# Performance work log

Measured on AMD Instinct MI355X. Metric: run time of the kernel, lower is better.

Reference implementation:

```python
import jax, jax.numpy as jnp
import numpy as np

N, E = 20000, 320000
NODE_DIM, EDGE_DIM, EMB, HEADS, HIDDEN, OUT = 128, 16, 128, 4, 512, 64
NEG_SLOPE = 0.2


def _gatv2(x, src0, dst0, ea, Wl, bl, Wr, br, We, att, bias):
    """PyG GATv2Conv (concat=True, add_self_loops=True, fill_value='mean')."""
    n = x.shape[0]
    e = src0.shape[0]
    H, C = att.shape
    # self loops; self-loop edge_attr = mean of incoming edge_attr per node (0 if none)
    cnt = jax.ops.segment_sum(jnp.ones((e,), x.dtype), dst0, num_segments=n)
    loop_attr = jax.ops.segment_sum(ea, dst0, num_segments=n) / jnp.maximum(cnt, 1.0)[:, None]
    loops = jnp.arange(n, dtype=src0.dtype)
    src = jnp.concatenate([src0, loops])
    dst = jnp.concatenate([dst0, loops])
    ea_full = jnp.concatenate([ea, loop_attr], axis=0)
    xl = (x @ Wl + bl).reshape(n, H, C)   # source transform
    xr = (x @ Wr + br).reshape(n, H, C)   # target transform
    ef = (ea_full @ We).reshape(-1, H, C)  # edge transform (no bias in PyG)
    s = jax.nn.leaky_relu(xl[src] + xr[dst] + ef, NEG_SLOPE)  # [E', H, C]
    logits = jnp.einsum('ehc,hc->eh', s, att)
    # scatter-softmax over incoming edges of each dst node (stable)
    mx = jax.ops.segment_max(logits, dst, num_segments=n)
    num = jnp.exp(logits - mx[dst])
    den = jax.ops.segment_sum(num, dst, num_segments=n)
    alpha = num / (den[dst] + 1e-16)
    out = jax.ops.segment_sum(alpha[:, :, None] * xl[src], dst, num_segments=n)
    return out.reshape(n, H * C) + bias


def _lin(key, fan_in, fan_out, dt=jnp.float32):
    return jax.random.normal(key, (fan_in, fan_out), dt) * (1.0 / np.sqrt(fan_in))


def setup_inputs() -> dict:
    key = jax.random.key(0)
    ks = jax.random.split(key, 24)
    HC = HEADS * EMB
    inp = {
        'x': jax.random.normal(ks[0], (N, NODE_DIM), jnp.float32),
        'edge_index': jax.random.randint(ks[1], (2, E), 0, N, jnp.int64),
        'edge_attr': jax.random.normal(ks[2], (E, EDGE_DIM), jnp.float32),
        # GATv2 layer 1
        'Wl1': _lin(ks[3], NODE_DIM, HC), 'bl1': jnp.zeros((HC,), jnp.float32),
        'Wr1': _lin(ks[4], NODE_DIM, HC), 'br1': jnp.zeros((HC,), jnp.float32),
        'We1': _lin(ks[5], EDGE_DIM, HC),
        'att1': jax.random.normal(ks[6], (HEADS, EMB), jnp.float32) * (1.0 / np.sqrt(EMB)),
        'bias1': jnp.zeros((HC,), jnp.float32),
        # GATv2 layer 2
        'Wl2': _lin(ks[7], HC, HC), 'bl2': jnp.zeros((HC,), jnp.float32),
        'Wr2': _lin(ks[8], HC, HC), 'br2': jnp.zeros((HC,), jnp.float32),
        'We2': _lin(ks[9], EDGE_DIM, HC),
        'att2': jax.random.normal(ks[10], (HEADS, EMB), jnp.float32) * (1.0 / np.sqrt(EMB)),
        'bias2': jnp.zeros((HC,), jnp.float32),
        # decoder MLP
        'Wd1': _lin(ks[11], HC, HIDDEN), 'bd1': jnp.zeros((HIDDEN,), jnp.float32),
        'Wd2': _lin(ks[12], HIDDEN, OUT), 'bd2': jnp.zeros((OUT,), jnp.float32),
    }
    return inp


def reference(x, edge_index, edge_attr,
              Wl1, bl1, Wr1, br1, We1, att1, bias1,
              Wl2, bl2, Wr2, br2, We2, att2, bias2,
              Wd1, bd1, Wd2, bd2):
    src, dst = edge_index[0], edge_index[1]
    h = _gatv2(x, src, dst, edge_attr, Wl1, bl1, Wr1, br1, We1, att1, bias1)
    h = _gatv2(h, src, dst, edge_attr, Wl2, bl2, Wr2, br2, We2, att2, bias2)
    q = jax.nn.relu(h @ Wd1 + bd1) @ Wd2 + bd2
    return q
```

## Files before the change

kernel.cpp:

```cpp
#include <hip/hip_runtime.h>
#include <hip/hip_fp16.h>

typedef _Float16 half8 __attribute__((ext_vector_type(8)));
typedef _Float16 half4 __attribute__((ext_vector_type(4)));
typedef _Float16 half2v __attribute__((ext_vector_type(2)));
typedef float f32x4 __attribute__((ext_vector_type(4)));

#if __has_builtin(__builtin_amdgcn_fdot2)
#define FDOT2(a, b, c) __builtin_amdgcn_fdot2((a), (b), (c), false)
#else
static __device__ __forceinline__ float FDOT2(half2v a, half2v b, float c) {
  return (float)a[0] * (float)b[0] + (float)a[1] * (float)b[1] + c;
}
#endif
#define H2(v8, p) ((half2v){(v8)[2 * (p)], (v8)[2 * (p) + 1]})

#define GLOAD_LDS16(gp, lp)                                                        \
  __builtin_amdgcn_global_load_lds(                                                \
      (const __attribute__((address_space(1))) void*)(gp),                         \
      (__attribute__((address_space(3))) void*)(lp), 16, 0, 0)

template <int CTRL>
__device__ __forceinline__ float dpp_add16(float x) {
  int y = __builtin_amdgcn_update_dpp(0, __float_as_int(x), CTRL, 0xf, 0xf, true);
  return x + __int_as_float(y);
}
__device__ __forceinline__ float rowsum16(float x) {
  x = dpp_add16<0x128>(x);
  x = dpp_add16<0x124>(x);
  x = dpp_add16<0x122>(x);
  x = dpp_add16<0x121>(x);
  return x;
}

__global__ void prep_kernel(const float* __restrict__ x, _Float16* __restrict__ x16, int nx,
                            const float* __restrict__ Wl1, const float* __restrict__ Wr1,
                            _Float16* __restrict__ WlrT1,
                            const float* __restrict__ Wl2, const float* __restrict__ Wr2,
                            _Float16* __restrict__ WlrT2,
                            const float* __restrict__ Wd1, _Float16* __restrict__ WdT1,
                            const float* __restrict__ Wd2, _Float16* __restrict__ WdT2,
                            const float* __restrict__ We1, _Float16* __restrict__ WeF1,
                            const float* __restrict__ We2, _Float16* __restrict__ WeF2,
                            const float* __restrict__ att1, _Float16* __restrict__ att16_1,
                            const float* __restrict__ att2, _Float16* __restrict__ att16_2,
                            const int* __restrict__ dst0, int* __restrict__ deg, int E) {
  int i = blockIdx.x * 256 + threadIdx.x;
  if (i < nx) { x16[i] = (_Float16)x[i]; return; }
  i -= nx;
  if (i < 1024 * 128) {
    int n = i >> 7, k = i & 127;
    float v = (n < 512) ? Wl1[(size_t)k * 512 + n] : Wr1[(size_t)k * 512 + (n - 512)];
    WlrT1[i] = (_Float16)v; return;
  }
  i -= 1024 * 128;
  if (i < 1024 * 512) {
    int n = i >> 9, k = i & 511;
    float v = (n < 512) ? Wl2[(size_t)k * 512 + n] : Wr2[(size_t)k * 512 + (n - 512)];
    WlrT2[i] = (_Float16)v; return;
  }
  i -= 1024 * 512;
  if (i < 512 * 512) { int n = i >> 9, k = i & 511; WdT1[i] = (_Float16)Wd1[(size_t)k * 512 + n]; return; }
  i -= 512 * 512;
  if (i < 64 * 512)  { int n = i >> 9, k = i & 511; WdT2[i] = (_Float16)Wd2[(size_t)k * 64 + n]; return; }
  i -= 64 * 512;
  if (i < 512 * 16) {
    int k = i & 15, c = (i >> 4) & 15, g = i >> 8;
    WeF1[i] = (_Float16)We1[(size_t)k * 512 + g * 16 + c]; return;
  }
  i -= 512 * 16;
  if (i < 512 * 16) {
    int k = i & 15, c = (i >> 4) & 15, g = i >> 8;
    WeF2[i] = (_Float16)We2[(size_t)k * 512 + g * 16 + c]; return;
  }
  i -= 512 * 16;
  if (i < 512)       { att16_1[i] = (_Float16)att1[i]; return; }
  i -= 512;
  if (i < 512)       { att16_2[i] = (_Float16)att2[i]; return; }
  i -= 512;
  if (i < E)         { atomicAdd(&deg[dst0[i]], 1); return; }
}

__global__ __launch_bounds__(1024) void scan_kernel(const int* __restrict__ deg, int* __restrict__ offs, int N) {
  __shared__ int part[1024];
  int t = threadIdx.x;
  int chunk = (N + 1023) / 1024;
  int b = t * chunk, e = min(b + chunk, N);
  int s = 0;
  for (int i = b; i < e; i++) s += deg[i] + 1;
  part[t] = s;
  __syncthreads();
  for (int off = 1; off < 1024; off <<= 1) {
    int v = (t >= off) ? part[t - off] : 0;
    __syncthreads();
    part[t] += v;
    __syncthreads();
  }
  int run = (t == 0) ? 0 : part[t - 1];
  for (int i = b; i < e; i++) { offs[i] = run; run += deg[i] + 1; }
  if (t == 1023) offs[N] = part[1023];
}

__global__ void csr_fill_kernel(const int* __restrict__ src0, const int* __restrict__ dst0,
                                const float* __restrict__ ea,
                                const int* __restrict__ offs, const int* __restrict__ deg,
                                int* __restrict__ cnt, int* __restrict__ csr_src,
                                _Float16* __restrict__ eas, int E, int N) {
  int i = blockIdx.x * 256 + threadIdx.x;
  if (i < 64) {
    if (i < 16) csr_src[E + N + i] = 0;
#pragma unroll
    for (int k = 0; k < 16; k++) eas[(size_t)(E + N + i) * 16 + k] = (_Float16)0.f;
  }
  if (i < E) {
    int d = dst0[i];
    int p = offs[d] + atomicAdd(&cnt[d], 1);
    csr_src[p] = src0[i];
    const float* s = ea + (size_t)i * 16;
    half8 h0, h1;
#pragma unroll
    for (int k = 0; k < 8; k++) { h0[k] = (_Float16)s[k]; h1[k] = (_Float16)s[k + 8]; }
    *(half8*)(eas + (size_t)p * 16) = h0;
    *(half8*)(eas + (size_t)p * 16 + 8) = h1;
  } else if (i < E + N) {
    int v = i - E;
    csr_src[offs[v] + deg[v]] = v;
  }
}

__global__ void loop_attr_kernel(const int* __restrict__ offs, const int* __restrict__ deg,
                                 _Float16* __restrict__ eas, int N) {
  int wid = (blockIdx.x * 256 + threadIdx.x) >> 6;
  int l = threadIdx.x & 63;
  if (wid >= N) return;
  int b = offs[wid], dg = deg[wid];
  int k = l & 15, r = l >> 4;
  float s = 0.f;
  for (int j = r; j < dg; j += 4)
    s += (float)eas[(size_t)(b + j) * 16 + k];
  s += __shfl_xor(s, 16, 64);
  s += __shfl_xor(s, 32, 64);
  if (r == 0) eas[(size_t)(b + dg) * 16 + k] = (_Float16)(s / fmaxf((float)dg, 1.0f));
}

template <bool RELU, bool OUT_F32>
__global__ __launch_bounds__(256) void gemm_f16(const _Float16* __restrict__ A,
                                                const _Float16* __restrict__ BT,
                                                const float* __restrict__ biasA,
                                                const float* __restrict__ biasB,
                                                void* __restrict__ C,
                                                int M, int K, int Nfull, int ldc) {
  __shared__ _Float16 As[128 * 32];
  __shared__ _Float16 Bs[128 * 32];
  int t = threadIdx.x;
  int m0 = blockIdx.x * 128;
  int n0 = blockIdx.y * 128;
  int l = t & 63, w = t >> 6;
  int wm = w & 1, wn = w >> 1;
  int lr = l & 15, lq = l >> 4;

  f32x4 acc[4][4];
#pragma unroll
  for (int i = 0; i < 4; i++)
#pragma unroll
    for (int j = 0; j < 4; j++) acc[i][j] = (f32x4){0.f, 0.f, 0.f, 0.f};

  int r0 = w * 32 + (l >> 2);
  int cb = (l & 3) * 8;
  const _Float16* Ap = A + (size_t)(m0 + r0) * K + cb;
  const _Float16* Bp = BT + (size_t)(n0 + r0) * K + cb;
  _Float16* AsW = As + w * 32 * 32;
  _Float16* BsW = Bs + w * 32 * 32;

  for (int kk = 0; kk < K; kk += 32) {
    GLOAD_LDS16(Ap, AsW);
    GLOAD_LDS16(Ap + (size_t)16 * K, AsW + 16 * 32);
    GLOAD_LDS16(Bp, BsW);
    GLOAD_LDS16(Bp + (size_t)16 * K, BsW + 16 * 32);
    Ap += 32; Bp += 32;
    __syncthreads();
    half8 af[4], bf[4];
#pragma unroll
    for (int mi = 0; mi < 4; mi++) af[mi] = *(const half8*)&As[(wm * 64 + mi * 16 + lr) * 32 + lq * 8];
#pragma unroll
    for (int ni = 0; ni < 4; ni++) bf[ni] = *(const half8*)&Bs[(wn * 64 + ni * 16 + lr) * 32 + lq * 8];
#pragma unroll
    for (int mi = 0; mi < 4; mi++)
#pragma unroll
      for (int ni = 0; ni < 4; ni++)
        acc[mi][ni] = __builtin_amdgcn_mfma_f32_16x16x32_f16(af[mi], bf[ni], acc[mi][ni], 0, 0, 0);
    __syncthreads();
  }

#pragma unroll
  for (int ni = 0; ni < 4; ni++) {
    int col = n0 + wn * 64 + ni * 16 + lr;
    if (col >= Nfull) continue;
    float bv = (col < 512) ? biasA[col] : biasB[col - 512];
#pragma unroll
    for (int mi = 0; mi < 4; mi++) {
#pragma unroll
      for (int r = 0; r < 4; r++) {
        int row = m0 + wm * 64 + mi * 16 + lq * 4 + r;
        if (row >= M) continue;
        float v = acc[mi][ni][r] + bv;
        if (RELU) v = fmaxf(v, 0.f);
        if (OUT_F32) ((float*)C)[(size_t)row * ldc + col] = v;
        else ((_Float16*)C)[(size_t)row * ldc + col] = (_Float16)v;
      }
    }
  }
}


__device__ __forceinline__ void upd(float p, half8 xs, float& m, float& den, float acc[8]) {
  float mn = fmaxf(m, p);
  float sc = __expf(m - mn);
  float al = __expf(p - mn);
  den = den * sc + al;
#pragma unroll
  for (int jj = 0; jj < 8; jj++) acc[jj] = acc[jj] * sc + al * (float)xs[jj];
  m = mn;
}

__global__ __launch_bounds__(256) void gat_fused_kernel(
    const _Float16* __restrict__ xlr,
    const int* __restrict__ csr_src, const int* __restrict__ offs,
    const _Float16* __restrict__ eas,
    const _Float16* __restrict__ WeF,
    const _Float16* __restrict__ att16,
    const float* __restrict__ bias,
    _Float16* __restrict__ hout, int N) {
  __shared__ _Float16 WeFL[16 * 512];
  __shared__ _Float16 EFs[4][16 * 512];
  int t = threadIdx.x;
  int l = t & 63;
  int w = t >> 6;
  int h = l >> 4;
  int c0 = l * 8;
  int lr = l & 15, lq = l >> 4;

  {
    const _Float16* gW = WeF + w * 512 + l * 8;
    _Float16* lW = WeFL + w * 512;
#pragma unroll
    for (int p = 0; p < 4; p++) GLOAD_LDS16(gW + p * 2048, lW + p * 2048);
  }
  __syncthreads();

  _Float16* EFw = &EFs[w][0];
  half8 attv = *(const half8*)(att16 + h * 128 + lr * 8);
  const half2v lk = {(_Float16)0.2f, (_Float16)0.2f};

  int wid = blockIdx.x * 4 + w;
  int nw = gridDim.x * 4;

  for (int v0 = wid; v0 < N; v0 += nw) {
    int v = __builtin_amdgcn_readfirstlane(v0);
    int b = offs[v], e2 = offs[v + 1];
    half8 xrv = *(const half8*)(xlr + (size_t)v * 1024 + 512 + c0);

    int s0 = csr_src[b], s1 = csr_src[b + 1], s2 = csr_src[b + 2], s3 = csr_src[b + 3];
    half8 xs0 = *(const half8*)(xlr + (size_t)s0 * 1024 + c0);
    half8 xs1 = *(const half8*)(xlr + (size_t)s1 * 1024 + c0);
    half8 xs2 = *(const half8*)(xlr + (size_t)s2 * 1024 + c0);
    half8 xs3 = *(const half8*)(xlr + (size_t)s3 * 1024 + c0);
    int t0 = csr_src[b + 4], t1 = csr_src[b + 5], t2 = csr_src[b + 6], t3 = csr_src[b + 7];
    half4 bfrag = *(const half4*)(eas + (size_t)(b + lr) * 16 + lq * 4);

    float m = -1e30f, den = 0.f;
    float acc[8];
#pragma unroll
    for (int j = 0; j < 8; j++) acc[j] = 0.f;

    for (int cs = b; cs < e2; cs += 16) {
#pragma unroll
      for (int g = 0; g < 32; g++) {
        half4 af = *(const half4*)(WeFL + g * 256 + lr * 16 + lq * 4);
        f32x4 d = __builtin_amdgcn_mfma_f32_16x16x16f16(af, bfrag, (f32x4){0.f, 0.f, 0.f, 0.f}, 0, 0, 0);
        half4 hd = {(_Float16)d[0], (_Float16)d[1], (_Float16)d[2], (_Float16)d[3]};
        int hi = (lr * 512 + g * 16 + lq * 4) ^ ((lr & 7) << 3);
        *(half4*)(EFw + hi) = hd;
      }
      bfrag = *(const half4*)(eas + (size_t)(cs + 16 + lr) * 16 + lq * 4);

      int cse = min(cs + 16, e2);
      for (int j = cs; j < cse; j += 4) {
        half8 nx0 = *(const half8*)(xlr + (size_t)t0 * 1024 + c0);
        half8 nx1 = *(const half8*)(xlr + (size_t)t1 * 1024 + c0);
        half8 nx2 = *(const half8*)(xlr + (size_t)t2 * 1024 + c0);
        half8 nx3 = *(const half8*)(xlr + (size_t)t3 * 1024 + c0);
        int u0 = csr_src[j + 8], u1 = csr_src[j + 9], u2 = csr_src[j + 10], u3 = csr_src[j + 11];

        int si = j - cs;
        half8 ef0 = *(const half8*)(EFw + (((si    ) * 512 + l * 8) ^ (((si    ) & 7) << 3)));
        half8 ef1 = *(const half8*)(EFw + (((si + 1) * 512 + l * 8) ^ (((si + 1) & 7) << 3)));
        half8 ef2 = *(const half8*)(EFw + (((si + 2) * 512 + l * 8) ^ (((si + 2) & 7) << 3)));
        half8 ef3 = *(const half8*)(EFw + (((si + 3) * 512 + l * 8) ^ (((si + 3) & 7) << 3)));

        float p0 = 0.f, p1 = 0.f, p2 = 0.f, p3 = 0.f;
#pragma unroll
        for (int p = 0; p < 4; p++) {
          half2v xrp = H2(xrv, p);
          half2v ap = H2(attv, p);
          half2v v0v = H2(xs0, p) + xrp + H2(ef0, p);
          half2v v1v = H2(xs1, p) + xrp + H2(ef1, p);
          half2v v2v = H2(xs2, p) + xrp + H2(ef2, p);
          half2v v3v = H2(xs3, p) + xrp + H2(ef3, p);
          v0v = __builtin_elementwise_max(v0v, v0v * lk);
          v1v = __builtin_elementwise_max(v1v, v1v * lk);
          v2v = __builtin_elementwise_max(v2v, v2v * lk);
          v3v = __builtin_elementwise_max(v3v, v3v * lk);
          p0 = FDOT2(v0v, ap, p0);
          p1 = FDOT2(v1v, ap, p1);
          p2 = FDOT2(v2v, ap, p2);
          p3 = FDOT2(v3v, ap, p3);
        }
        p0 = rowsum16(p0); p1 = rowsum16(p1); p2 = rowsum16(p2); p3 = rowsum16(p3);

        upd(p0, xs0, m, den, acc);
        if (j + 1 < e2) upd(p1, xs1, m, den, acc);
        if (j + 2 < e2) upd(p2, xs2, m, den, acc);
        if (j + 3 < e2) upd(p3, xs3, m, den, acc);

        xs0 = nx0; xs1 = nx1; xs2 = nx2; xs3 = nx3;
        t0 = u0; t1 = u1; t2 = u2; t3 = u3;
      }
    }
    float rd = 1.f / (den + 1e-16f);
    half8 o;
#pragma unroll
    for (int jj = 0; jj < 8; jj++) o[jj] = (_Float16)(fmaf(acc[jj], rd, bias[c0 + jj]));
    *(half8*)(hout + (size_t)v * 512 + c0) = o;
  }
}


extern "C" void kernel_launch(void* const* d_in, const int* in_sizes, int n_in,
                              void* d_out, int out_size, void* d_ws, size_t ws_size,
                              hipStream_t stream) {
  (void)n_in; (void)out_size; (void)ws_size;
  const float* x    = (const float*)d_in[0];
  const int*   ei   = (const int*)d_in[1];
  const float* ea   = (const float*)d_in[2];
  const float* Wl1  = (const float*)d_in[3];
  const float* bl1  = (const float*)d_in[4];
  const float* Wr1  = (const float*)d_in[5];
  const float* br1  = (const float*)d_in[6];
  const float* We1  = (const float*)d_in[7];
  const float* att1 = (const float*)d_in[8];
  const float* bias1= (const float*)d_in[9];
  const float* Wl2  = (const float*)d_in[10];
  const float* bl2  = (const float*)d_in[11];
  const float* Wr2  = (const float*)d_in[12];
  const float* br2  = (const float*)d_in[13];
  const float* We2  = (const float*)d_in[14];
  const float* att2 = (const float*)d_in[15];
  const float* bias2= (const float*)d_in[16];
  const float* Wd1  = (const float*)d_in[17];
  const float* bd1  = (const float*)d_in[18];
  const float* Wd2  = (const float*)d_in[19];
  const float* bd2  = (const float*)d_in[20];

  const int N = in_sizes[0] / 128;
  const int E = in_sizes[1] / 2;
  const int EP = E + N;
  const int Npad = (N + 127) & ~127;
  const int* src0 = ei;
  const int* dst0 = ei + E;

  char* ws = (char*)d_ws;
  size_t off = 0;
  auto alloc = [&](size_t bytes) -> void* {
    void* p = ws + off;
    off += (bytes + 255) & ~(size_t)255;
    return p;
  };

  int*   deg    = (int*)alloc((size_t)N * 8);
  int*   cnt    = deg + N;
  int*   offs   = (int*)alloc(((size_t)N + 1) * 4);
  int*   csr_src= (int*)alloc(((size_t)EP + 16) * 4);
  _Float16* eas = (_Float16*)alloc(((size_t)EP + 64) * 16 * 2);
  _Float16* x16   = (_Float16*)alloc((size_t)Npad * 128 * 2);
  _Float16* xlr16 = (_Float16*)alloc((size_t)Npad * 1024 * 2);
  _Float16* h16   = (_Float16*)alloc((size_t)Npad * 512 * 2);
  _Float16* WlrT1 = (_Float16*)alloc(1024 * 128 * 2);
  _Float16* WlrT2 = (_Float16*)alloc(1024 * 512 * 2);
  _Float16* WdT1  = (_Float16*)alloc(512 * 512 * 2);
  _Float16* WdT2  = (_Float16*)alloc(128 * 512 * 2);
  _Float16* WeF1  = (_Float16*)alloc(16 * 512 * 2);
  _Float16* WeF2  = (_Float16*)alloc(16 * 512 * 2);
  _Float16* att16_1 = (_Float16*)alloc(512 * 2);
  _Float16* att16_2 = (_Float16*)alloc(512 * 2);
  _Float16* t16   = xlr16;

  hipMemsetAsync(deg, 0, (size_t)N * 8, stream);

  int nx = N * 128;
  int prep_base = nx + 1024 * 128 + 1024 * 512 + 512 * 512 + 64 * 512
                + 512 * 16 + 512 * 16 + 512 + 512;
  int prep_total = prep_base + E;
  prep_kernel<<<(prep_total + 255) / 256, 256, 0, stream>>>(
      x, x16, nx, Wl1, Wr1, WlrT1, Wl2, Wr2, WlrT2,
      Wd1, WdT1, Wd2, WdT2, We1, WeF1, We2, WeF2,
      att1, att16_1, att2, att16_2, dst0, deg, E);

  int g;
  scan_kernel<<<1, 1024, 0, stream>>>(deg, offs, N);
  g = (EP + 255) / 256;
  csr_fill_kernel<<<g, 256, 0, stream>>>(src0, dst0, ea, offs, deg, cnt, csr_src, eas, E, N);
  g = (N * 64 + 255) / 256;
  loop_attr_kernel<<<g, 256, 0, stream>>>(offs, deg, eas, N);

  dim3 gb(256);
  dim3 ggm((N + 127) / 128, 8);
  dim3 ggd((N + 127) / 128, 4);
  dim3 ggo((N + 127) / 128, 1);

  const int FGRID = 2048;

  gemm_f16<false, false><<<ggm, gb, 0, stream>>>(x16, WlrT1, bl1, br1, xlr16, N, 128, 1024, 1024);
  gat_fused_kernel<<<FGRID, 256, 0, stream>>>(xlr16, csr_src, offs, eas, WeF1, att16_1, bias1, h16, N);

  gemm_f16<false, false><<<ggm, gb, 0, stream>>>(h16, WlrT2, bl2, br2, xlr16, N, 512, 1024, 1024);
  gat_fused_kernel<<<FGRID, 256, 0, stream>>>(xlr16, csr_src, offs, eas, WeF2, att16_2, bias2, h16, N);

  gemm_f16<true, false><<<ggd, gb, 0, stream>>>(h16, WdT1, bd1, bd1, t16, N, 512, 512, 512);
  gemm_f16<false, true><<<ggo, gb, 0, stream>>>(t16, WdT2, bd2, bd2, d_out, N, 512, 64, 64);
}
```

Measured before the change: 509.1 us.

## Deepen gather prefetch pipeline across nodes and batch online-softmax updates

The fused GAT kernel now prefetches the next node's CSR offsets, source indices, target features and first gathered rows while the current node is being processed. Within a node the source-row gathers run two groups of four edges ahead instead of one. The four per-edge online-softmax updates are merged into a single rescale per group of four, and the We fragment layout is permuted so the MFMA A-operand load is a contiguous lane-indexed read. The grid is cut from 2048 to 512 blocks so each wave handles more nodes and the cross-node prefetch has work to hide behind, at the cost of more registers and lower occupancy.

```diff
diff --git a/kernel.cpp b/kernel.cpp
--- a/kernel.cpp
+++ b/kernel.cpp
@@ -65,13 +65,15 @@
   if (i < 64 * 512)  { int n = i >> 9, k = i & 511; WdT2[i] = (_Float16)Wd2[(size_t)k * 64 + n]; return; }
   i -= 64 * 512;
   if (i < 512 * 16) {
-    int k = i & 15, c = (i >> 4) & 15, g = i >> 8;
-    WeF1[i] = (_Float16)We1[(size_t)k * 512 + g * 16 + c]; return;
+    int j = i & 3, lrow = (i >> 2) & 63, g = i >> 8;
+    int lq = lrow >> 4, lrr = lrow & 15;
+    WeF1[i] = (_Float16)We1[(size_t)(lq * 4 + j) * 512 + g * 16 + lrr]; return;
   }
   i -= 512 * 16;
   if (i < 512 * 16) {
-    int k = i & 15, c = (i >> 4) & 15, g = i >> 8;
-    WeF2[i] = (_Float16)We2[(size_t)k * 512 + g * 16 + c]; return;
+    int j = i & 3, lrow = (i >> 2) & 63, g = i >> 8;
+    int lq = lrow >> 4, lrr = lrow & 15;
+    WeF2[i] = (_Float16)We2[(size_t)(lq * 4 + j) * 512 + g * 16 + lrr]; return;
   }
   i -= 512 * 16;
   if (i < 512)       { att16_1[i] = (_Float16)att1[i]; return; }
@@ -212,16 +214,6 @@
   }
 }
 
-
-__device__ __forceinline__ void upd(float p, half8 xs, float& m, float& den, float acc[8]) {
-  float mn = fmaxf(m, p);
-  float sc = __expf(m - mn);
-  float al = __expf(p - mn);
-  den = den * sc + al;
-#pragma unroll
-  for (int jj = 0; jj < 8; jj++) acc[jj] = acc[jj] * sc + al * (float)xs[jj];
-  m = mn;
-}
 
 __global__ __launch_bounds__(256) void gat_fused_kernel(
     const _Float16* __restrict__ xlr,
@@ -255,18 +247,51 @@
   int wid = blockIdx.x * 4 + w;
   int nw = gridDim.x * 4;
 
+  int bN = 0, eN = 0;
+  int sAn0 = 0, sAn1 = 0, sAn2 = 0, sAn3 = 0;
+  int sBn0 = 0, sBn1 = 0, sBn2 = 0, sBn3 = 0;
+  int sCn0 = 0, sCn1 = 0, sCn2 = 0, sCn3 = 0;
+  half8 xrvn = {}, gAn0 = {}, gAn1 = {}, gAn2 = {}, gAn3 = {};
+  half4 bfn = {};
+  if (wid < N) {
+    bN = offs[wid]; eN = offs[wid + 1];
+    sAn0 = csr_src[bN]; sAn1 = csr_src[bN + 1]; sAn2 = csr_src[bN + 2]; sAn3 = csr_src[bN + 3];
+    sBn0 = csr_src[bN + 4]; sBn1 = csr_src[bN + 5]; sBn2 = csr_src[bN + 6]; sBn3 = csr_src[bN + 7];
+    sCn0 = csr_src[bN + 8]; sCn1 = csr_src[bN + 9]; sCn2 = csr_src[bN + 10]; sCn3 = csr_src[bN + 11];
+    xrvn = *(const half8*)(xlr + (size_t)wid * 1024 + 512 + c0);
+    gAn0 = *(const half8*)(xlr + (size_t)sAn0 * 1024 + c0);
+    gAn1 = *(const half8*)(xlr + (size_t)sAn1 * 1024 + c0);
+    gAn2 = *(const half8*)(xlr + (size_t)sAn2 * 1024 + c0);
+    gAn3 = *(const half8*)(xlr + (size_t)sAn3 * 1024 + c0);
+    bfn = *(const half4*)(eas + (size_t)(bN + lr) * 16 + lq * 4);
+  }
+
   for (int v0 = wid; v0 < N; v0 += nw) {
-    int v = __builtin_amdgcn_readfirstlane(v0);
-    int b = offs[v], e2 = offs[v + 1];
-    half8 xrv = *(const half8*)(xlr + (size_t)v * 1024 + 512 + c0);
-
-    int s0 = csr_src[b], s1 = csr_src[b + 1], s2 = csr_src[b + 2], s3 = csr_src[b + 3];
-    half8 xs0 = *(const half8*)(xlr + (size_t)s0 * 1024 + c0);
-    half8 xs1 = *(const half8*)(xlr + (size_t)s1 * 1024 + c0);
-    half8 xs2 = *(const half8*)(xlr + (size_t)s2 * 1024 + c0);
-    half8 xs3 = *(const half8*)(xlr + (size_t)s3 * 1024 + c0);
-    int t0 = csr_src[b + 4], t1 = csr_src[b + 5], t2 = csr_src[b + 6], t3 = csr_src[b + 7];
-    half4 bfrag = *(const half4*)(eas + (size_t)(b + lr) * 16 + lq * 4);
+    int b = bN, e2 = eN;
+    half8 xrv = xrvn;
+    half8 xs0 = gAn0, xs1 = gAn1, xs2 = gAn2, xs3 = gAn3;
+    int t0 = sBn0, t1 = sBn1, t2 = sBn2, t3 = sBn3;
+    int u0 = sCn0, u1 = sCn1, u2 = sCn2, u3 = sCn3;
+    half4 bfrag = bfn;
+
+    int vn = v0 + nw;
+    if (vn < N) {
+      bN = offs[vn]; eN = offs[vn + 1];
+      sAn0 = csr_src[bN]; sAn1 = csr_src[bN + 1]; sAn2 = csr_src[bN + 2]; sAn3 = csr_src[bN + 3];
+      sBn0 = csr_src[bN + 4]; sBn1 = csr_src[bN + 5]; sBn2 = csr_src[bN + 6]; sBn3 = csr_src[bN + 7];
+      sCn0 = csr_src[bN + 8]; sCn1 = csr_src[bN + 9]; sCn2 = csr_src[bN + 10]; sCn3 = csr_src[bN + 11];
+      xrvn = *(const half8*)(xlr + (size_t)vn * 1024 + 512 + c0);
+      gAn0 = *(const half8*)(xlr + (size_t)sAn0 * 1024 + c0);
+      gAn1 = *(const half8*)(xlr + (size_t)sAn1 * 1024 + c0);
+      gAn2 = *(const half8*)(xlr + (size_t)sAn2 * 1024 + c0);
+      gAn3 = *(const half8*)(xlr + (size_t)sAn3 * 1024 + c0);
+      bfn = *(const half4*)(eas + (size_t)(bN + lr) * 16 + lq * 4);
+    }
+
+    half8 gB0 = *(const half8*)(xlr + (size_t)t0 * 1024 + c0);
+    half8 gB1 = *(const half8*)(xlr + (size_t)t1 * 1024 + c0);
+    half8 gB2 = *(const half8*)(xlr + (size_t)t2 * 1024 + c0);
+    half8 gB3 = *(const half8*)(xlr + (size_t)t3 * 1024 + c0);
 
     float m = -1e30f, den = 0.f;
     float acc[8];
@@ -274,23 +299,28 @@
     for (int j = 0; j < 8; j++) acc[j] = 0.f;
 
     for (int cs = b; cs < e2; cs += 16) {
+      half4 nbfrag = *(const half4*)(eas + (size_t)(cs + 16 + lr) * 16 + lq * 4);
+
 #pragma unroll
       for (int g = 0; g < 32; g++) {
-        half4 af = *(const half4*)(WeFL + g * 256 + lr * 16 + lq * 4);
+        half4 af = *(const half4*)(WeFL + g * 256 + l * 4);
         f32x4 d = __builtin_amdgcn_mfma_f32_16x16x16f16(af, bfrag, (f32x4){0.f, 0.f, 0.f, 0.f}, 0, 0, 0);
         half4 hd = {(_Float16)d[0], (_Float16)d[1], (_Float16)d[2], (_Float16)d[3]};
         int hi = (lr * 512 + g * 16 + lq * 4) ^ ((lr & 7) << 3);
         *(half4*)(EFw + hi) = hd;
       }
-      bfrag = *(const half4*)(eas + (size_t)(cs + 16 + lr) * 16 + lq * 4);
+      bfrag = nbfrag;
 
       int cse = min(cs + 16, e2);
       for (int j = cs; j < cse; j += 4) {
-        half8 nx0 = *(const half8*)(xlr + (size_t)t0 * 1024 + c0);
-        half8 nx1 = *(const half8*)(xlr + (size_t)t1 * 1024 + c0);
-        half8 nx2 = *(const half8*)(xlr + (size_t)t2 * 1024 + c0);
-        half8 nx3 = *(const half8*)(xlr + (size_t)t3 * 1024 + c0);
-        int u0 = csr_src[j + 8], u1 = csr_src[j + 9], u2 = csr_src[j + 10], u3 = csr_src[j + 11];
+        half8 gC0, gC1, gC2, gC3;
+        if (j + 8 < e2) {
+          gC0 = *(const half8*)(xlr + (size_t)u0 * 1024 + c0);
+          gC1 = *(const half8*)(xlr + (size_t)u1 * 1024 + c0);
+          gC2 = *(const half8*)(xlr + (size_t)u2 * 1024 + c0);
+          gC3 = *(const half8*)(xlr + (size_t)u3 * 1024 + c0);
+        }
+        int n0i = csr_src[j + 12], n1i = csr_src[j + 13], n2i = csr_src[j + 14], n3i = csr_src[j + 15];
 
         int si = j - cs;
         half8 ef0 = *(const half8*)(EFw + (((si    ) * 512 + l * 8) ^ (((si    ) & 7) << 3)));
@@ -318,20 +348,32 @@
         }
         p0 = rowsum16(p0); p1 = rowsum16(p1); p2 = rowsum16(p2); p3 = rowsum16(p3);
 
-        upd(p0, xs0, m, den, acc);
-        if (j + 1 < e2) upd(p1, xs1, m, den, acc);
-        if (j + 2 < e2) upd(p2, xs2, m, den, acc);
-        if (j + 3 < e2) upd(p3, xs3, m, den, acc);
-
-        xs0 = nx0; xs1 = nx1; xs2 = nx2; xs3 = nx3;
-        t0 = u0; t1 = u1; t2 = u2; t3 = u3;
+        if (j + 1 >= e2) p1 = -1e30f;
+        if (j + 2 >= e2) p2 = -1e30f;
+        if (j + 3 >= e2) p3 = -1e30f;
+        float q = fmaxf(fmaxf(fmaxf(p0, p1), fmaxf(p2, p3)), m);
+        float sc = __expf(m - q);
+        float a0 = __expf(p0 - q), a1 = __expf(p1 - q);
+        float a2 = __expf(p2 - q), a3 = __expf(p3 - q);
+        den = den * sc + ((a0 + a1) + (a2 + a3));
+#pragma unroll
+        for (int jj = 0; jj < 8; jj++) {
+          float s0 = fmaf(a0, (float)xs0[jj], a1 * (float)xs1[jj]);
+          float s1 = fmaf(a2, (float)xs2[jj], a3 * (float)xs3[jj]);
+          acc[jj] = fmaf(acc[jj], sc, s0 + s1);
+        }
+        m = q;
+
+        xs0 = gB0; xs1 = gB1; xs2 = gB2; xs3 = gB3;
+        gB0 = gC0; gB1 = gC1; gB2 = gC2; gB3 = gC3;
+        u0 = n0i; u1 = n1i; u2 = n2i; u3 = n3i;
       }
     }
     float rd = 1.f / (den + 1e-16f);
     half8 o;
 #pragma unroll
     for (int jj = 0; jj < 8; jj++) o[jj] = (_Float16)(fmaf(acc[jj], rd, bias[c0 + jj]));
-    *(half8*)(hout + (size_t)v * 512 + c0) = o;
+    *(half8*)(hout + (size_t)v0 * 512 + c0) = o;
   }
 }
 
@@ -418,7 +460,7 @@
   dim3 ggd((N + 127) / 128, 4);
   dim3 ggo((N + 127) / 128, 1);
 
-  const int FGRID = 2048;
+  const int FGRID = 512;
 
   gemm_f16<false, false><<<ggm, gb, 0, stream>>>(x16, WlrT1, bl1, br1, xlr16, N, 128, 1024, 1024);
   gat_fused_kernel<<<FGRID, 256, 0, stream>>>(xlr16, csr_src, offs, eas, WeF1, att16_1, bias1, h16, N);
```

Result: slower. 587.4 us (+15.4%).
